# Performance work log

Measured on AMD Instinct MI355X. Metric: run time of the kernel, lower is better.

The kernel has to match this reference:

```python
import jax, jax.numpy as jnp
import numpy as np

TAU = 10.0
K = 5
EPS = 1e-8


def get_patches(x, k):
    # x: [B, C, H, W] -> [B, C, k, k, L] with L=(H-k+1)*(W-k+1), stride-1 sliding window
    B, C, H, W = x.shape
    Hp, Wp = H - k + 1, W - k + 1
    p = jnp.stack(
        [jnp.stack([x[:, :, i:i + Hp, j:j + Wp] for j in range(k)], axis=2) for i in range(k)],
        axis=2,
    )  # [B, C, k, k, Hp, Wp]
    return p.reshape(B, C, k, k, Hp * Wp)


def setup_inputs() -> dict:
    key = jax.random.key(0)
    k1, k2 = jax.random.split(key)
    semantic_features = jax.random.normal(k1, (2, 32, 192, 192), dtype=jnp.float32)
    depth_gt = jax.random.uniform(k2, (2, 1, 192, 192), dtype=jnp.float32)
    return {"semantic_features": semantic_features, "depth_gt": depth_gt}


def reference(semantic_features, depth_gt):
    k = K
    c = k // 2
    sp = get_patches(semantic_features, k)            # [B, C, k, k, L]
    dp = get_patches(1.0 / (depth_gt + 1e-6), k)      # [B, 1, k, k, L]
    sem_center = sp[:, :, c, c, :]                    # [B, C, L]
    depth_center = dp[:, 0, c, c, :]                  # [B, L]

    depth_diff = jnp.abs(depth_center[:, None, None, :] - dp[:, 0])           # [B, k, k, L]
    sem_diff = jnp.sqrt(jnp.sum((sem_center[:, :, None, None, :] - sp) ** 2, axis=1))  # [B, k, k, L]

    depth_diff = jnp.maximum(depth_diff, EPS)
    sem_diff = jnp.maximum(sem_diff, EPS)

    loss0 = (jnp.expm1(-depth_diff / TAU) + 1.0) * (jnp.expm1(-sem_diff ** 2) + 1.0)  # [B, k, k, L]

    m = (depth_diff > EPS) & (sem_diff > EPS)         # [B, k, k, L]
    pos = dp[:, 0] > 0.0                              # [B, k, k, L]
    # faithful to torch broadcasting: [B,k,k,L] & [B,1,k,k,L] -> [B,B,k,k,L]
    mask = m[None] & pos[:, None]                     # [B, B, k, k, L]
    loss = loss0[None] * mask.astype(loss0.dtype)     # [B, B, k, k, L]

    center_mask = jnp.ones((k, k), loss.dtype).at[c, c].set(0.0)
    loss = loss * center_mask[None, None, :, :, None]
    return jnp.mean(jnp.mean(loss, axis=(2, 3)))
```

## Files before the change

kernel.cpp:

```cpp
#include <hip/hip_runtime.h>
#include <math.h>


#define HP    188
#define IMW   192
#define NCH   32
#define TW    64
#define HWC   68
#define NR2   6
#define NYT   94
#define PLANE (IMW * IMW)
#define NWRK  (3 * NYT * 2)
#define NBLK  568
#define NSLOT (8 * NR2 * HWC)
#define SPT   13

__device__ __forceinline__ unsigned bf16_bits(float f) {
    unsigned u = __float_as_uint(f);
    return (u + 0x7fffu + ((u >> 16) & 1u)) >> 16;
}
__device__ __forceinline__ float bf16_rne(float f) {
    unsigned u = __float_as_uint(f);
    u += 0x7fffu + ((u >> 16) & 1u);
    u &= 0xffff0000u;
    return __uint_as_float(u);
}
__device__ __forceinline__ float lo_f(unsigned p) { return __uint_as_float(p << 16); }
__device__ __forceinline__ float hi_f(unsigned p) { return __uint_as_float(p & 0xffff0000u); }

__global__ __launch_bounds__(256) void dgp_tiled(
    const float* __restrict__ S,
    const float* __restrict__ D,
    double* __restrict__ partials)
{
    __shared__ __align__(8) uint2 smp[8][NR2][HWC];
    __shared__ float  rd[NR2][HWC];
    __shared__ double wsum[4];

    const int tid = threadIdx.x;
    const int tx  = tid & 63;
    const int tg  = tid >> 6;

    const int l   = blockIdx.x;
    const int xcd = l & 7;
    const int g   = xcd * 71 + (l >> 3);
    if (g >= NWRK) {
        if (tid == 0) partials[l] = 0.0;
        return;
    }
    const int c   = g / NYT;
    const int oy0 = (g - c * NYT) * 2;
    const int b   = c / 3;
    const int ox0 = (c - 3 * b) * TW;

    float dv[2];
#pragma unroll
    for (int s = 0; s < 2; ++s) {
        const int t = tid + 256 * s;
        float d = 1.0f;
        if (t < NR2 * HWC) {
            const int i   = t / HWC;
            const int col = t - i * HWC;
            const int gc  = ox0 + col;
            if (gc < IMW) d = D[(b * IMW + (oy0 + i)) * IMW + gc];
        }
        dv[s] = d;
    }
    float4 sv[SPT];
#pragma unroll
    for (int s = 0; s < SPT; ++s) {
        const int t = tid + 256 * s;
        float4 v = make_float4(0.f, 0.f, 0.f, 0.f);
        if (t < NSLOT) {
            const int q   = t / (NR2 * HWC);
            const int rem = t - q * (NR2 * HWC);
            const int i   = rem / HWC;
            const int col = rem - i * HWC;
            const int gc  = ox0 + col;
            if (gc < IMW) {
                const int base = ((b * NCH + 4 * q) * IMW + (oy0 + i)) * IMW + gc;
                v.x = S[base];
                v.y = S[base + PLANE];
                v.z = S[base + 2 * PLANE];
                v.w = S[base + 3 * PLANE];
            }
        }
        sv[s] = v;
    }

#pragma unroll
    for (int s = 0; s < 2; ++s) {
        const int t = tid + 256 * s;
        if (t < NR2 * HWC) {
            const int i   = t / HWC;
            const int col = t - i * HWC;
            rd[i][col] = 1.0f / (bf16_rne(dv[s]) + 1e-6f);
        }
    }
#pragma unroll
    for (int s = 0; s < SPT; ++s) {
        const int t = tid + 256 * s;
        if (t < NSLOT) {
            const int q   = t / (NR2 * HWC);
            const int rem = t - q * (NR2 * HWC);
            const int i   = rem / HWC;
            const int col = rem - i * HWC;
            const float4 v = sv[s];
            uint2 pk;
            pk.x = bf16_bits(v.x) | (__float_as_uint(bf16_rne(v.y)) & 0xffff0000u);
            pk.y = bf16_bits(v.z) | (__float_as_uint(bf16_rne(v.w)) & 0xffff0000u);
            smp[q][i][col] = pk;
        }
    }
    __syncthreads();

    double acc = 0.0;
    const int ox = ox0 + tx;
    if (ox < HP) {
#pragma unroll
        for (int py = 0; py < 2; ++py) {
            float cs[NCH];
#pragma unroll
            for (int q = 0; q < 8; ++q) {
                const uint2 p = smp[q][py + 2][tx + 2];
                cs[4 * q + 0] = lo_f(p.x);
                cs[4 * q + 1] = hi_f(p.x);
                cs[4 * q + 2] = lo_f(p.y);
                cs[4 * q + 3] = hi_f(p.y);
            }
            const float rc = rd[py + 2][tx + 2];

            for (int k = 0; k < 6; ++k) {
                int t = tg * 6 + k;
                t += (t >= 12);
                const int i = py + t / 5;
                const int j = t - 5 * (t / 5);

                float f0 = 0.f, f1 = 0.f, f2 = 0.f, f3 = 0.f;
#pragma unroll
                for (int q = 0; q < 8; ++q) {
                    const uint2 p = smp[q][i][tx + j];
                    const float t0 = cs[4 * q + 0] - lo_f(p.x);
                    const float t1 = cs[4 * q + 1] - hi_f(p.x);
                    const float t2 = cs[4 * q + 2] - lo_f(p.y);
                    const float t3 = cs[4 * q + 3] - hi_f(p.y);
                    f0 = fmaf(t0, t0, f0);
                    f1 = fmaf(t1, t1, f1);
                    f2 = fmaf(t2, t2, f2);
                    f3 = fmaf(t3, t3, f3);
                }
                const float sq_fast = (f0 + f1) + (f2 + f3);

                if (sq_fast <= 18.001f) {
                    const float rn = rd[i][tx + j];
                    const float dd = fabsf(rc - rn);

                    float r[8];
                    {
#pragma clang fp contract(off)
#pragma unroll
                        for (int blk = 0; blk < 4; ++blk) {
                            const uint2 pe = smp[2 * blk][i][tx + j];
                            const uint2 po = smp[2 * blk + 1][i][tx + j];
                            float p;
                            p = cs[8 * blk + 0] - lo_f(pe.x); p = p * p; r[0] = blk ? r[0] + p : p;
                            p = cs[8 * blk + 1] - hi_f(pe.x); p = p * p; r[1] = blk ? r[1] + p : p;
                            p = cs[8 * blk + 2] - lo_f(pe.y); p = p * p; r[2] = blk ? r[2] + p : p;
                            p = cs[8 * blk + 3] - hi_f(pe.y); p = p * p; r[3] = blk ? r[3] + p : p;
                            p = cs[8 * blk + 4] - lo_f(po.x); p = p * p; r[4] = blk ? r[4] + p : p;
                            p = cs[8 * blk + 5] - hi_f(po.x); p = p * p; r[5] = blk ? r[5] + p : p;
                            p = cs[8 * blk + 6] - lo_f(po.y); p = p * p; r[6] = blk ? r[6] + p : p;
                            p = cs[8 * blk + 7] - hi_f(po.y); p = p * p; r[7] = blk ? r[7] + p : p;
                        }
                    }
                    const float sq = ((r[0] + r[1]) + (r[2] + r[3]))
                                   + ((r[4] + r[5]) + (r[6] + r[7]));

                    const float sd  = sqrtf(sq);
                    const float ddc = fmaxf(dd, 1e-8f);
                    const float sdc = fmaxf(sd, 1e-8f);

                    if (ddc > 1e-8f && sdc > 1e-8f) {
                        const float s2 = sdc * sdc;
                        if (s2 <= 18.0f) {
                            const float ls = (float)expm1(-(double)s2) + 1.0f;
                            const float ad = -(ddc / 10.0f);
                            const float ld = (float)expm1((double)ad) + 1.0f;
                            acc += 2.0 * (double)(ld * ls);
                        }
                    }
                }
            }
        }
    }

#pragma unroll
    for (int off = 32; off > 0; off >>= 1)
        acc += __shfl_down(acc, off);
    if ((tid & 63) == 0) wsum[tid >> 6] = acc;
    __syncthreads();
    if (tid == 0)
        partials[l] = wsum[0] + wsum[1] + wsum[2] + wsum[3];
}

__global__ __launch_bounds__(256) void dgp_fin(
    const double* __restrict__ partials, float* __restrict__ out)
{
    const int tid = threadIdx.x;
    double acc = 0.0;
    for (int k = tid; k < NBLK; k += 256)
        acc += partials[k];
#pragma unroll
    for (int off = 32; off > 0; off >>= 1)
        acc += __shfl_down(acc, off);
    __shared__ double ws[4];
    if ((tid & 63) == 0) ws[tid >> 6] = acc;
    __syncthreads();
    if (tid == 0)
        out[0] = (float)((ws[0] + ws[1] + ws[2] + ws[3]) / 3534400.0);
}

extern "C" void kernel_launch(void* const* d_in, const int* in_sizes, int n_in,
                              void* d_out, int out_size, void* d_ws, size_t ws_size,
                              hipStream_t stream)
{
    const float* S = (const float*)d_in[0];
    const float* D = (const float*)d_in[1];
    if (n_in >= 2 && in_sizes[0] < in_sizes[1]) {
        S = (const float*)d_in[1];
        D = (const float*)d_in[0];
    }
    double* partials = (double*)d_ws;

    dgp_tiled<<<NBLK, 256, 0, stream>>>(S, D, partials);
    dgp_fin<<<1, 256, 0, stream>>>(partials, (float*)d_out);
}
```

Measured before the change: 73.46 us.

## Exploit symmetry of pairwise tap terms to halve neighbor evaluations

The pairwise term between a pixel and a neighbor at offset (di,dj) is symmetric, so each unordered pair is now evaluated once from one side with doubled weight. The mirror tap is only evaluated explicitly where the partner pixel falls outside the valid center region, near the borders. This removes roughly half of the 24-tap distance and exp work per pixel. In exchange it adds constant-memory tap tables and boundary weight logic, and correctness depends on the border weighting exactly matching the reference's set of valid centers.

```diff
diff --git a/kernel.cpp b/kernel.cpp
--- a/kernel.cpp
+++ b/kernel.cpp
@@ -27,6 +27,9 @@
 }
 __device__ __forceinline__ float lo_f(unsigned p) { return __uint_as_float(p << 16); }
 __device__ __forceinline__ float hi_f(unsigned p) { return __uint_as_float(p & 0xffff0000u); }
+
+__constant__ int HTI[12] = {2,2,3,3,3,3,3,4,4,4,4,4};
+__constant__ int HTJ[12] = {3,4,0,1,2,3,4,0,1,2,3,4};
 
 __global__ __launch_bounds__(256) void dgp_tiled(
     const float* __restrict__ S,
@@ -130,16 +133,11 @@
             }
             const float rc = rd[py + 2][tx + 2];
 
-            for (int k = 0; k < 6; ++k) {
-                int t = tg * 6 + k;
-                t += (t >= 12);
-                const int i = py + t / 5;
-                const int j = t - 5 * (t / 5);
-
+            auto eval_tap = [&](int i, int jc, float w) {
                 float f0 = 0.f, f1 = 0.f, f2 = 0.f, f3 = 0.f;
 #pragma unroll
                 for (int q = 0; q < 8; ++q) {
-                    const uint2 p = smp[q][i][tx + j];
+                    const uint2 p = smp[q][i][jc];
                     const float t0 = cs[4 * q + 0] - lo_f(p.x);
                     const float t1 = cs[4 * q + 1] - hi_f(p.x);
                     const float t2 = cs[4 * q + 2] - lo_f(p.y);
@@ -152,16 +150,15 @@
                 const float sq_fast = (f0 + f1) + (f2 + f3);
 
                 if (sq_fast <= 18.001f) {
-                    const float rn = rd[i][tx + j];
+                    const float rn = rd[i][jc];
                     const float dd = fabsf(rc - rn);
-
                     float r[8];
                     {
 #pragma clang fp contract(off)
 #pragma unroll
                         for (int blk = 0; blk < 4; ++blk) {
-                            const uint2 pe = smp[2 * blk][i][tx + j];
-                            const uint2 po = smp[2 * blk + 1][i][tx + j];
+                            const uint2 pe = smp[2 * blk][i][jc];
+                            const uint2 po = smp[2 * blk + 1][i][jc];
                             float p;
                             p = cs[8 * blk + 0] - lo_f(pe.x); p = p * p; r[0] = blk ? r[0] + p : p;
                             p = cs[8 * blk + 1] - hi_f(pe.x); p = p * p; r[1] = blk ? r[1] + p : p;
@@ -175,21 +172,41 @@
                     }
                     const float sq = ((r[0] + r[1]) + (r[2] + r[3]))
                                    + ((r[4] + r[5]) + (r[6] + r[7]));
-
                     const float sd  = sqrtf(sq);
                     const float ddc = fmaxf(dd, 1e-8f);
                     const float sdc = fmaxf(sd, 1e-8f);
-
                     if (ddc > 1e-8f && sdc > 1e-8f) {
                         const float s2 = sdc * sdc;
                         if (s2 <= 18.0f) {
                             const float ls = (float)expm1(-(double)s2) + 1.0f;
                             const float ad = -(ddc / 10.0f);
                             const float ld = (float)expm1((double)ad) + 1.0f;
-                            acc += 2.0 * (double)(ld * ls);
+                            acc += (double)w * (double)(ld * ls);
                         }
                     }
                 }
+            };
+
+#pragma unroll
+            for (int m = 0; m < 3; ++m) {
+                const int t  = tg * 3 + m;
+                const int ti = HTI[t];
+                const int tj = HTJ[t];
+
+                const int i1    = py + ti;
+                const int j1    = tx + tj;
+                const int t1row = oy0 + i1;
+                const int t1col = ox0 + j1;
+                const float w1  = (t1row <= 189 && t1col >= 2 && t1col <= 189)
+                                ? 4.0f : 2.0f;
+                eval_tap(i1, j1, w1);
+
+                const int i2    = py + 4 - ti;
+                const int j2    = tx + 4 - tj;
+                const int t2row = oy0 + i2;
+                const int t2col = ox0 + j2;
+                if (t2row < 2 || t2col < 2 || t2col > 189)
+                    eval_tap(i2, j2, 2.0f);
             }
         }
     }
```

Result: faster. 71.54 us (-2.6%).
